# Optimization experiments

Hardware: AMD Instinct MI355X
Metric: run time of the kernel (lower is better)

## Reference

```python
import jax, jax.numpy as jnp
import numpy as np

N = 25600            # 64 graphs x 400 ROIs
F_IN = 400
H = 128
E = 512000           # 8000 edges per graph
B = 64
G = 8
OUT = 2
NPG = 400            # nodes per graph
EPG = E // B         # edges per graph
BN_EPS = 1e-5


def _xavier(k, shape):
    lim = float(np.sqrt(6.0 / (shape[0] + shape[1])))
    return jax.random.uniform(k, shape, jnp.float32, -lim, lim)


def setup_inputs() -> dict:
    key = jax.random.key(0)
    ks = jax.random.split(key, 16)
    inp = {}
    inp["x"] = jax.random.normal(ks[0], (N, F_IN), jnp.float32)
    # within-graph random edges: local index + graph offset
    src_l = jax.random.randint(ks[1], (E,), 0, NPG, jnp.int32)
    dst_l = jax.random.randint(ks[2], (E,), 0, NPG, jnp.int32)
    off = (jnp.arange(E, dtype=jnp.int32) // EPG) * NPG
    inp["edge_index"] = jnp.stack([src_l + off, dst_l + off])
    inp["batch"] = (jnp.arange(N, dtype=jnp.int32) // NPG)
    inp["group_ids"] = jax.random.randint(ks[3], (N,), 0, G, jnp.int32)
    inp["ge"] = _xavier(ks[4], (G, 2))
    inp["he"] = _xavier(ks[5], (2, 2))
    dims = [(F_IN + 4, H), (H, H), (H, H)]
    for i, (di, do) in enumerate(dims):
        k1, k2 = jax.random.split(ks[6 + i])
        inp[f"w{i}a"] = _xavier(k1, (di, do))
        inp[f"b{i}a"] = jnp.zeros((do,), jnp.float32)
        inp[f"g{i}"] = jnp.ones((do,), jnp.float32)
        inp[f"be{i}"] = jnp.zeros((do,), jnp.float32)
        inp[f"w{i}b"] = _xavier(k2, (do, do))
        inp[f"b{i}b"] = jnp.zeros((do,), jnp.float32)
    inp["wfa"] = _xavier(ks[10], (H, H))
    inp["bfa"] = jnp.zeros((H,), jnp.float32)
    inp["wfb"] = _xavier(ks[11], (H, OUT))
    inp["bfb"] = jnp.zeros((OUT,), jnp.float32)
    return inp


def _bn(h, gamma, beta):
    # BatchNorm1d in training mode: stats over node dimension
    mu = jnp.mean(h, axis=0, keepdims=True)
    var = jnp.var(h, axis=0, keepdims=True)
    return gamma * (h - mu) * jax.lax.rsqrt(var + BN_EPS) + beta


def reference(x, edge_index, batch, group_ids, ge, he,
              w0a, b0a, g0, be0, w0b, b0b,
              w1a, b1a, g1, be1, w1b, b1b,
              w2a, b2a, g2, be2, w2b, b2b,
              wfa, bfa, wfb, bfb):
    n = x.shape[0]
    hemi = jnp.arange(n) % 2                      # [1::2] = 1
    h = jnp.concatenate([x, ge[group_ids], he[hemi]], axis=-1)  # [N, F_IN+4]
    src, dst = edge_index[0], edge_index[1]
    layers = [(w0a, b0a, g0, be0, w0b, b0b),
              (w1a, b1a, g1, be1, w1b, b1b),
              (w2a, b2a, g2, be2, w2b, b2b)]
    for wa, ba, g, be, wb, bb in layers:
        # GINConv (eps=0): x_i + sum_{(j,i)} x_j, then 2-layer MLP w/ batchnorm
        agg = jax.ops.segment_sum(h[src], dst, num_segments=N)
        z = h + agg
        z = jax.nn.relu(_bn(z @ wa + ba, g, be))  # dropout = identity (eval)
        h = jax.nn.relu(z @ wb + bb)              # outer ReLU from forward()
    pooled = jax.ops.segment_sum(h, batch, num_segments=B)  # global_add_pool
    return jax.nn.relu(pooled @ wfa + bfa) @ wfb + bfb
```

## Files before the change

### kernel.cpp

```cpp
#include <hip/hip_runtime.h>

#define N_NODES 25600
#define F_IN 400
#define NE 512000
#define NB 64
#define NPG 400
#define EPG 8000
#define BN_EPS 1e-5f
#define NBLK 256

typedef __attribute__((ext_vector_type(8))) short short8;
typedef __attribute__((ext_vector_type(4))) float floatx4;
typedef unsigned short us;
typedef unsigned long long u64;

__device__ __forceinline__ unsigned short f2bf(float f) {
    unsigned int u = __float_as_uint(f);
    u += 0x7FFF + ((u >> 16) & 1);
    return (unsigned short)(u >> 16);
}
__device__ __forceinline__ float bf2f(unsigned short s) {
    return __uint_as_float((unsigned int)s << 16);
}
__device__ __forceinline__ short u8bf(unsigned v) {
    return (short)(__float_as_uint((float)v) >> 16);
}
__device__ __forceinline__ void ast64(void* p, u64 v) {
    __hip_atomic_store((u64*)p, v, __ATOMIC_RELAXED, __HIP_MEMORY_SCOPE_AGENT);
}
__device__ __forceinline__ u64 pk4(unsigned short a, unsigned short b, unsigned short c, unsigned short d) {
    return (u64)a | ((u64)b << 16) | ((u64)c << 32) | ((u64)d << 48);
}

__device__ __forceinline__ void gsync_tree(unsigned* bar, int bid, int phase) {
    __syncthreads();
    if (threadIdx.x == 0) {
        unsigned* leaf = bar + 32 + (bid >> 4) * 32;
        unsigned v = __hip_atomic_fetch_add(leaf, 1u, __ATOMIC_RELAXED, __HIP_MEMORY_SCOPE_AGENT);
        if (v == (unsigned)(phase * 16 - 1))
            __hip_atomic_fetch_add(bar, 1u, __ATOMIC_RELAXED, __HIP_MEMORY_SCOPE_AGENT);
        while (__hip_atomic_load(bar, __ATOMIC_RELAXED, __HIP_MEMORY_SCOPE_AGENT) < (unsigned)(phase * 16))
            __builtin_amdgcn_s_sleep(16);
        asm volatile("" ::: "memory");
    }
    __syncthreads();
}

__device__ __forceinline__ void gbar4(unsigned* gc, int stage) {
    __syncthreads();
    if (threadIdx.x == 0) {
        __hip_atomic_fetch_add(gc, 1u, __ATOMIC_RELAXED, __HIP_MEMORY_SCOPE_AGENT);
        while (__hip_atomic_load(gc, __ATOMIC_RELAXED, __HIP_MEMORY_SCOPE_AGENT) < (unsigned)(stage * 4))
            __builtin_amdgcn_s_sleep(8);
        asm volatile("" ::: "memory");
    }
    __syncthreads();
}



__device__ __forceinline__ void ph_prep(unsigned char* sm, int g, int q, int bid, int tid,
        const int* __restrict__ src, const int* __restrict__ dst, us* __restrict__ SbBF,
        const float* __restrict__ wa0, const float* __restrict__ wa1, const float* __restrict__ wa2,
        const float* __restrict__ wb0, const float* __restrict__ wb1, const float* __restrict__ wb2,
        us* __restrict__ wt0, us* __restrict__ wtb0, us* __restrict__ wta1,
        us* __restrict__ wtb1, us* __restrict__ wta2, us* __restrict__ wtb2,
        float* __restrict__ pstat, us* __restrict__ tT0, us* __restrict__ tT1, us* __restrict__ tT2) {
    int r0 = q * 112;
    int* cnt = (int*)sm;
    for (int i = tid; i < 11200; i += 1024) cnt[i] = 0;
    __syncthreads();
    int ebase = g * EPG, nbase = g * NPG;
    for (int e = tid; e < EPG; e += 1024) {
        int d = dst[ebase + e] - nbase;
        int dr = d - r0;
        if ((unsigned)dr < 112u) {
            int s = src[ebase + e] - nbase;
            int idx = dr * NPG + s;
            atomicAdd(&cnt[idx >> 2], (int)(1u << ((idx & 3) * 8)));
        }
    }
    __syncthreads();
    const unsigned char* cb = (const unsigned char*)cnt;
    for (int i = tid; i < 112 * 112; i += 1024) {
        int rr = i / 112, c4 = (i % 112) * 4;
        int R = r0 + rr;
        ushort4 o;
#pragma unroll
        for (int j = 0; j < 4; ++j) {
            int c = c4 + j;
            unsigned v = (R < NPG && c < NPG) ? (unsigned)cb[rr * NPG + c] + (c == R ? 1u : 0u) : 0u;
            ((unsigned short*)&o)[j] = (unsigned short)u8bf(v);
        }
        *(ushort4*)&SbBF[((size_t)g * 512 + R) * 448 + c4] = o;
    }
    if (q == 3) {
        for (int i = tid; i < 64 * 112; i += 1024) {
            int rr = 448 + i / 112, c4 = (i % 112) * 4;
            *(u64*)&SbBF[((size_t)g * 512 + rr) * 448 + c4] = 0ull;
        }
    }
    if (bid < 64) {
        int idx = bid * 1024 + tid;
        if (idx < 14336) {
            int n = idx / 112, k0 = (idx % 112) * 4;
            unsigned short o[4];
#pragma unroll
            for (int j = 0; j < 4; ++j) {
                int k = k0 + j;
                o[j] = (k < 400) ? f2bf(wa0[(size_t)k * 128 + n]) : (unsigned short)0;
            }
            ast64(&wt0[(size_t)n * 448 + k0], pk4(o[0], o[1], o[2], o[3]));
        } else if (idx < 34816) {
            int r2 = idx - 14336;
            int m = r2 >> 12, qi = r2 & 4095;
            int r = qi * 4, n = r >> 7, k = r & 127;
            const float* smat = (m == 0) ? wb0 : (m == 1) ? wa1 : (m == 2) ? wb1 : (m == 3) ? wa2 : wb2;
            us* dmat = (m == 0) ? wtb0 : (m == 1) ? wta1 : (m == 2) ? wtb1 : (m == 3) ? wta2 : wtb2;
            unsigned short o[4];
#pragma unroll
            for (int j = 0; j < 4; ++j) o[j] = f2bf(smat[(size_t)(k + j) * 128 + n]);
            ast64(&dmat[r], pk4(o[0], o[1], o[2], o[3]));
        } else if (idx < 45056) {
            int qi = idx - 34816;
            ast64(&((u64*)pstat)[qi], 0ull);
        } else if (idx < 45440) {
            int qi = idx - 45056;
            us* t = (qi < 128) ? tT0 : (qi < 256) ? tT1 : tT2;
            ast64(&t[(size_t)128 * N_NODES + (qi & 127) * 4], 0ull);
        }
    }
}


__device__ __forceinline__ void ph_embed(unsigned char* sm, int g, int q, int tid,
        const float* __restrict__ x, const us* __restrict__ wt0, const float* __restrict__ wa0,
        const int* __restrict__ gid, const float* __restrict__ ge, const float* __restrict__ he,
        us* __restrict__ tTw) {
    us (*Bf)[456] = (us(*)[456])sm;
    us (*As)[72] = (us(*)[72])(sm + 116736);
    float (*Wex)[128] = (float(*)[128])(sm + 135168);
    int nb = g * NPG + q * 100;
    int wave = tid >> 6, lane = tid & 63;
    int wrow = wave >> 2, wc4 = wave & 3;
    int fm = lane & 15, quad = lane >> 4;

    for (int i = tid; i < 7168; i += 1024) {
        int col = i / 56, kq = (i % 56) * 8;
        *(short8*)&Bf[col][kq] = *(const short8*)(wt0 + (size_t)col * 448 + kq);
    }
    for (int i = tid; i < 512; i += 1024)
        Wex[i >> 7][i & 127] = wa0[(size_t)(400 + (i >> 7)) * 128 + (i & 127)];

    floatx4 acc[2][2];
#pragma unroll
    for (int rt = 0; rt < 2; ++rt)
#pragma unroll
        for (int ct = 0; ct < 2; ++ct) acc[rt][ct] = (floatx4){0.f, 0.f, 0.f, 0.f};

    const int rA = tid >> 3, kcA = (tid & 7) * 8;
    float v[8];
    auto loadK = [&](int ks) {
        int kg = ks * 64 + kcA;
        if (rA < 100) {
            const float* ar = x + (size_t)(nb + rA) * F_IN;
            if (kg + 7 < 400) {
                float4 a = *(const float4*)(ar + kg);
                float4 b = *(const float4*)(ar + kg + 4);
                v[0] = a.x; v[1] = a.y; v[2] = a.z; v[3] = a.w;
                v[4] = b.x; v[5] = b.y; v[6] = b.z; v[7] = b.w;
            } else {
#pragma unroll
                for (int j = 0; j < 8; ++j) v[j] = (kg + j < 400) ? ar[kg + j] : 0.f;
            }
        } else {
#pragma unroll
            for (int j = 0; j < 8; ++j) v[j] = 0.f;
        }
    };

    loadK(0);
    for (int ks = 0; ks < 7; ++ks) {
        {
            short8 s;
#pragma unroll
            for (int j = 0; j < 8; ++j) s[j] = (short)f2bf(v[j]);
            *(short8*)&As[rA][kcA] = s;
        }
        __syncthreads();
        if (ks + 1 < 7) loadK(ks + 1);
#pragma unroll
        for (int k0l = 0; k0l < 64; k0l += 32) {
            short8 af[2], bf[2];
#pragma unroll
            for (int rt = 0; rt < 2; ++rt)
                af[rt] = *(const short8*)&As[wrow * 32 + rt * 16 + fm][k0l + quad * 8];
#pragma unroll
            for (int ct = 0; ct < 2; ++ct)
                bf[ct] = *(const short8*)&Bf[wc4 * 32 + ct * 16 + fm][ks * 64 + k0l + quad * 8];
#pragma unroll
            for (int rt = 0; rt < 2; ++rt)
#pragma unroll
                for (int ct = 0; ct < 2; ++ct)
                    acc[rt][ct] = __builtin_amdgcn_mfma_f32_16x16x32_bf16(
                        af[rt], bf[ct], acc[rt][ct], 0, 0, 0);
        }
        __syncthreads();
    }

#pragma unroll
    for (int rt = 0; rt < 2; ++rt)
#pragma unroll
        for (int ct = 0; ct < 2; ++ct) {
            int col = wc4 * 32 + ct * 16 + fm;
            int rl0 = wrow * 32 + rt * 16 + quad * 4;
            if (rl0 < 100) {
                unsigned short o[4];
#pragma unroll
                for (int r = 0; r < 4; ++r) {
                    int row = nb + rl0 + r;
                    int gv = gid[row];
                    float vv = acc[rt][ct][r]
                             + ge[gv * 2] * Wex[0][col] + ge[gv * 2 + 1] * Wex[1][col]
                             + he[(row & 1) * 2] * Wex[2][col] + he[(row & 1) * 2 + 1] * Wex[3][col];
                    o[r] = f2bf(vv);
                }
                ast64(&tTw[(size_t)col * N_NODES + nb + rl0], pk4(o[0], o[1], o[2], o[3]));
            }
        }
}


__device__ __forceinline__ void ph_agg(unsigned char* sm, int g, int q, int tid,
        const us* __restrict__ SbBF, const us* __restrict__ tTr, const float* __restrict__ ba,
        float* __restrict__ psum, float* __restrict__ psq, int bucket) {
    us (*Bf)[456] = (us(*)[456])sm;
    us (*zl)[136] = (us(*)[136])sm;
    float (*rs)[4][2][16] = (float(*)[4][2][16])(sm + 116736);
    float (*rq)[4][2][16] = (float(*)[4][2][16])(sm + 118784);
    int wave = tid >> 6, lane = tid & 63;
    int wrow = wave >> 2, wc4 = wave & 3;
    int fm = lane & 15, quad = lane >> 4;
    int node0 = g * NPG;

    for (int i = tid; i < 7168; i += 1024) {
        int col = i / 56, kq = (i % 56) * 8;
        *(short8*)&Bf[col][kq] = *(const short8*)(tTr + (size_t)col * N_NODES + node0 + kq);
    }
    __syncthreads();

    floatx4 acc[2][2];
#pragma unroll
    for (int rt = 0; rt < 2; ++rt)
#pragma unroll
        for (int ct = 0; ct < 2; ++ct) acc[rt][ct] = (floatx4){0.f, 0.f, 0.f, 0.f};

    const us* abase = SbBF + ((size_t)g * 512 + q * 112) * 448;
#pragma unroll
    for (int ks = 0; ks < 7; ++ks) {
#pragma unroll
        for (int k0l = 0; k0l < 64; k0l += 32) {
            short8 af[2], bf[2];
#pragma unroll
            for (int rt = 0; rt < 2; ++rt)
                af[rt] = *(const short8*)(abase + (size_t)(wrow * 32 + rt * 16 + fm) * 448
                                          + ks * 64 + k0l + quad * 8);
#pragma unroll
            for (int ct = 0; ct < 2; ++ct)
                bf[ct] = *(const short8*)&Bf[wc4 * 32 + ct * 16 + fm][ks * 64 + k0l + quad * 8];
#pragma unroll
            for (int rt = 0; rt < 2; ++rt)
#pragma unroll
                for (int ct = 0; ct < 2; ++ct)
                    acc[rt][ct] = __builtin_amdgcn_mfma_f32_16x16x32_bf16(
                        af[rt], bf[ct], acc[rt][ct], 0, 0, 0);
        }
    }
    __syncthreads();

    int nrows = (q < 3) ? 112 : 64;
    float sc[2] = {0.f, 0.f}, sq2[2] = {0.f, 0.f};
#pragma unroll
    for (int rt = 0; rt < 2; ++rt)
#pragma unroll
        for (int ct = 0; ct < 2; ++ct) {
            int col = wc4 * 32 + ct * 16 + fm;
            int rl0 = wrow * 32 + rt * 16 + quad * 4;
            if (rl0 < nrows) {
                float bv = ba[col];
#pragma unroll
                for (int r = 0; r < 4; ++r) {
                    float vv = acc[rt][ct][r] + bv;
                    zl[rl0 + r][col] = f2bf(vv);
                    sc[ct] += vv;
                    sq2[ct] += vv * vv;
                }
            }
        }
#pragma unroll
    for (int ct = 0; ct < 2; ++ct) {
        sc[ct] += __shfl_xor(sc[ct], 16);
        sc[ct] += __shfl_xor(sc[ct], 32);
        sq2[ct] += __shfl_xor(sq2[ct], 16);
        sq2[ct] += __shfl_xor(sq2[ct], 32);
    }
    if (lane < 16) {
#pragma unroll
        for (int ct = 0; ct < 2; ++ct) { rs[wrow][wc4][ct][lane] = sc[ct]; rq[wrow][wc4][ct][lane] = sq2[ct]; }
    }
    __syncthreads();
    if (tid < 128) {
        int wc = tid >> 5, ct = (tid >> 4) & 1, f = tid & 15;
        float S = 0.f, Q = 0.f;
#pragma unroll
        for (int wr = 0; wr < 4; ++wr) { S += rs[wr][wc][ct][f]; Q += rq[wr][wc][ct][f]; }
        atomicAdd(&psum[bucket * 128 + tid], S);
        atomicAdd(&psq[bucket * 128 + tid], Q);
    }
}


template <int FINAL>
__device__ __forceinline__ void ph_post(unsigned char* sm, int g, int q, int tid,
        const float* __restrict__ psum, const float* __restrict__ psq,
        const float* __restrict__ gamma, const float* __restrict__ beta,
        const us* __restrict__ wtb, const float* __restrict__ bb,
        const us* __restrict__ wta_next, us* __restrict__ tTw, float& p0, float& p1) {
    us (*zl)[136] = (us(*)[136])sm;
    float* coefs = (float*)(sm + 34816);
    us (*hs)[136] = (us(*)[136])(sm + 35840);
    us (*Bw)[72] = (us(*)[72])(sm + 70656);
    int wave = tid >> 6, lane = tid & 63;
    int wrow = wave >> 2, wc4 = wave & 3;
    int fm = lane & 15, quad = lane >> 4;
    int nrows = (q < 3) ? 112 : 64;
    int nb = g * NPG + q * 112;

    if (tid < 128) {
        float S = 0.f, Q = 0.f;
#pragma unroll
        for (int b = 0; b < 16; ++b) {
            S += __hip_atomic_load(&psum[b * 128 + tid], __ATOMIC_RELAXED, __HIP_MEMORY_SCOPE_AGENT);
            Q += __hip_atomic_load(&psq[b * 128 + tid], __ATOMIC_RELAXED, __HIP_MEMORY_SCOPE_AGENT);
        }
        float invn = 1.0f / (float)N_NODES;
        float mu = S * invn;
        float var = Q * invn - mu * mu;
        float a = gamma[tid] * rsqrtf(var + BN_EPS);
        coefs[tid] = a;
        coefs[128 + tid] = beta[tid] - a * mu;
    }
    __syncthreads();
    for (int i = tid; i < 16384; i += 1024) {
        int rl = i >> 7, col = i & 127;
        float vv = bf2f(zl[rl][col]);
        zl[rl][col] = f2bf(fmaxf(coefs[col] * vv + coefs[128 + col], 0.f));
    }
    __syncthreads();

    floatx4 acc[2][2];
#pragma unroll
    for (int rt = 0; rt < 2; ++rt)
#pragma unroll
        for (int ct = 0; ct < 2; ++ct) acc[rt][ct] = (floatx4){0.f, 0.f, 0.f, 0.f};

    const int nB = tid >> 3, kc = (tid & 7) * 8;
    for (int ks = 0; ks < 2; ++ks) {
        *(short8*)&Bw[nB][kc] = *(const short8*)(wtb + (size_t)nB * 128 + ks * 64 + kc);
        __syncthreads();
#pragma unroll
        for (int k0l = 0; k0l < 64; k0l += 32) {
            short8 af[2], bf[2];
#pragma unroll
            for (int rt = 0; rt < 2; ++rt)
                af[rt] = *(const short8*)&zl[wrow * 32 + rt * 16 + fm][ks * 64 + k0l + quad * 8];
#pragma unroll
            for (int ct = 0; ct < 2; ++ct)
                bf[ct] = *(const short8*)&Bw[wc4 * 32 + ct * 16 + fm][k0l + quad * 8];
#pragma unroll
            for (int rt = 0; rt < 2; ++rt)
#pragma unroll
                for (int ct = 0; ct < 2; ++ct)
                    acc[rt][ct] = __builtin_amdgcn_mfma_f32_16x16x32_bf16(
                        af[rt], bf[ct], acc[rt][ct], 0, 0, 0);
        }
        __syncthreads();
    }

    if (FINAL) {
#pragma unroll
        for (int rt = 0; rt < 2; ++rt)
#pragma unroll
            for (int ct = 0; ct < 2; ++ct) {
                int col = wc4 * 32 + ct * 16 + fm;
                int rl0 = wrow * 32 + rt * 16 + quad * 4;
                if (rl0 < nrows) {
                    float bv = bb[col];
                    float s = 0.f;
#pragma unroll
                    for (int r = 0; r < 4; ++r) s += fmaxf(acc[rt][ct][r] + bv, 0.f);
                    if (ct == 0) p0 += s; else p1 += s;
                }
            }
        return;
    }

#pragma unroll
    for (int rt = 0; rt < 2; ++rt)
#pragma unroll
        for (int ct = 0; ct < 2; ++ct) {
            int col = wc4 * 32 + ct * 16 + fm;
            float bv = bb[col];
            int rl0 = wrow * 32 + rt * 16 + quad * 4;
#pragma unroll
            for (int r = 0; r < 4; ++r)
                hs[rl0 + r][col] = f2bf(fmaxf(acc[rt][ct][r] + bv, 0.f));
        }
    __syncthreads();

#pragma unroll
    for (int rt = 0; rt < 2; ++rt)
#pragma unroll
        for (int ct = 0; ct < 2; ++ct) acc[rt][ct] = (floatx4){0.f, 0.f, 0.f, 0.f};

    for (int ks = 0; ks < 2; ++ks) {
        *(short8*)&Bw[nB][kc] = *(const short8*)(wta_next + (size_t)nB * 128 + ks * 64 + kc);
        __syncthreads();
#pragma unroll
        for (int k0l = 0; k0l < 64; k0l += 32) {
            short8 af[2], bf[2];
#pragma unroll
            for (int rt = 0; rt < 2; ++rt)
                af[rt] = *(const short8*)&hs[wrow * 32 + rt * 16 + fm][ks * 64 + k0l + quad * 8];
#pragma unroll
            for (int ct = 0; ct < 2; ++ct)
                bf[ct] = *(const short8*)&Bw[wc4 * 32 + ct * 16 + fm][k0l + quad * 8];
#pragma unroll
            for (int rt = 0; rt < 2; ++rt)
#pragma unroll
                for (int ct = 0; ct < 2; ++ct)
                    acc[rt][ct] = __builtin_amdgcn_mfma_f32_16x16x32_bf16(
                        af[rt], bf[ct], acc[rt][ct], 0, 0, 0);
        }
        __syncthreads();
    }

#pragma unroll
    for (int rt = 0; rt < 2; ++rt)
#pragma unroll
        for (int ct = 0; ct < 2; ++ct) {
            int col = wc4 * 32 + ct * 16 + fm;
            int rl0 = wrow * 32 + rt * 16 + quad * 4;
            if (rl0 < nrows) {
                unsigned short o[4];
#pragma unroll
                for (int r = 0; r < 4; ++r) o[r] = f2bf(acc[rt][ct][r]);
                ast64(&tTw[(size_t)col * N_NODES + nb + rl0], pk4(o[0], o[1], o[2], o[3]));
            }
        }
}


__global__ __launch_bounds__(1024, 4) void persist_all(
        const float* __restrict__ x, const int* __restrict__ esrc, const int* __restrict__ edst,
        const int* __restrict__ gid, const float* __restrict__ ge, const float* __restrict__ he,
        const float* __restrict__ wa0, const float* __restrict__ ba0, const float* __restrict__ gg0,
        const float* __restrict__ be0, const float* __restrict__ wb0, const float* __restrict__ bbias0,
        const float* __restrict__ wa1, const float* __restrict__ ba1, const float* __restrict__ gg1,
        const float* __restrict__ be1, const float* __restrict__ wb1, const float* __restrict__ bbias1,
        const float* __restrict__ wa2, const float* __restrict__ ba2, const float* __restrict__ gg2,
        const float* __restrict__ be2, const float* __restrict__ wb2, const float* __restrict__ bbias2,
        const float* __restrict__ wfa, const float* __restrict__ bfa,
        const float* __restrict__ wfb, const float* __restrict__ bfb,
        us* __restrict__ tT0, us* __restrict__ tT1, us* __restrict__ tT2,
        us* __restrict__ SbBF, float* __restrict__ pstat,
        us* __restrict__ wt0, us* __restrict__ wtb0, us* __restrict__ wta1,
        us* __restrict__ wtb1, us* __restrict__ wta2, us* __restrict__ wtb2,
        unsigned* __restrict__ bar, float* __restrict__ out) {
    __shared__ __align__(16) unsigned char sm[137216];
    int bid = blockIdx.x, tid = threadIdx.x;
    int g = (bid & 7) * 8 + ((bid >> 3) & 7);
    int q = bid >> 6;
    unsigned* gc = bar + 544 + g * 32;
    float* pooled = pstat + 12288;
    float p0 = 0.f, p1 = 0.f;

    ph_prep(sm, g, q, bid, tid, esrc, edst, SbBF, wa0, wa1, wa2, wb0, wb1, wb2,
            wt0, wtb0, wta1, wtb1, wta2, wtb2, pstat, tT0, tT1, tT2);
    gsync_tree(bar, bid, 1);
    ph_embed(sm, g, q, tid, x, wt0, wa0, gid, ge, he, tT0);
    gbar4(gc, 1);

    ph_agg(sm, g, q, tid, SbBF, tT0, ba0, pstat + 0, pstat + 2048, bid & 15);
    gsync_tree(bar, bid, 2);
    ph_post<0>(sm, g, q, tid, pstat + 0, pstat + 2048, gg0, be0, wtb0, bbias0, wta1, tT1, p0, p1);
    gbar4(gc, 2);

    ph_agg(sm, g, q, tid, SbBF, tT1, ba1, pstat + 4096, pstat + 6144, bid & 15);
    gsync_tree(bar, bid, 3);
    ph_post<0>(sm, g, q, tid, pstat + 4096, pstat + 6144, gg1, be1, wtb1, bbias1, wta2, tT2, p0, p1);
    gbar4(gc, 3);

    ph_agg(sm, g, q, tid, SbBF, tT2, ba2, pstat + 8192, pstat + 10240, bid & 15);
    gsync_tree(bar, bid, 4);
    ph_post<1>(sm, g, q, tid, pstat + 8192, pstat + 10240, gg2, be2, wtb2, bbias2, nullptr, nullptr, p0, p1);

    {
        int wave = tid >> 6, lane = tid & 63;
        int wrow = wave >> 2, wc4 = wave & 3;
        float (*red)[4][2][16] = (float(*)[4][2][16])sm;
        p0 += __shfl_xor(p0, 16); p0 += __shfl_xor(p0, 32);
        p1 += __shfl_xor(p1, 16); p1 += __shfl_xor(p1, 32);
        __syncthreads();
        if (lane < 16) { red[wrow][wc4][0][lane] = p0; red[wrow][wc4][1][lane] = p1; }
        __syncthreads();
        if (tid < 128) {
            int wc = tid >> 5, ct = (tid >> 4) & 1, f = tid & 15;
            float s = 0.f;
#pragma unroll
            for (int wr = 0; wr < 4; ++wr) s += red[wr][wc][ct][f];
            atomicAdd(&pooled[g * 128 + tid], s);
        }
    }
    gbar4(gc, 4);

    if (q == 0) {
        float* pl = (float*)sm;
        float* o0 = pl + 128;
        float* o1 = pl + 256;
        __syncthreads();
        if (tid < 128) {
            unsigned uv = __hip_atomic_load((const unsigned*)&pooled[g * 128 + tid],
                                            __ATOMIC_RELAXED, __HIP_MEMORY_SCOPE_AGENT);
            pl[tid] = __uint_as_float(uv);
        }
        __syncthreads();
        if (tid < 128) {
            float a = bfa[tid];
            for (int k = 0; k < 128; ++k) a += pl[k] * wfa[k * 128 + tid];
            float p2 = fmaxf(a, 0.f);
            o0[tid] = p2 * wfb[tid * 2 + 0];
            o1[tid] = p2 * wfb[tid * 2 + 1];
        }
        __syncthreads();
        if (tid == 0) {
            float a0 = bfb[0], a1 = bfb[1];
#pragma unroll
            for (int k = 0; k < 128; ++k) { a0 += o0[k]; a1 += o1[k]; }
            out[g * 2 + 0] = a0;
            out[g * 2 + 1] = a1;
        }
    }
}


extern "C" void kernel_launch(void* const* d_in, const int* in_sizes, int n_in,
                              void* d_out, int out_size, void* d_ws, size_t ws_size,
                              hipStream_t stream) {
    const float* x   = (const float*)d_in[0];
    const int* ei    = (const int*)d_in[1];
    const int* gid   = (const int*)d_in[3];
    const float* ge  = (const float*)d_in[4];
    const float* he  = (const float*)d_in[5];
    float* out = (float*)d_out;

    char* ws = (char*)d_ws;
    size_t o = 0;
    auto alloc = [&](size_t bytes) { char* p = ws + o; o += (bytes + 255) & ~(size_t)255; return p; };
    size_t tbytes = ((size_t)128 * N_NODES + 512) * 2;
    us* tT0 = (us*)alloc(tbytes);
    us* tT1 = (us*)alloc(tbytes);
    us* tT2 = (us*)alloc(tbytes);
    us* SbBF = (us*)alloc((size_t)NB * 512 * 448 * 2);
    float* pstat = (float*)alloc(20480 * 4);
    us* wt0  = (us*)alloc(128 * 448 * 2);
    us* wtb0 = (us*)alloc(128 * 128 * 2);
    us* wta1 = (us*)alloc(128 * 128 * 2);
    us* wtb1 = (us*)alloc(128 * 128 * 2);
    us* wta2 = (us*)alloc(128 * 128 * 2);
    us* wtb2 = (us*)alloc(128 * 128 * 2);
    unsigned* bar = (unsigned*)alloc(12288);
    (void)ws_size; (void)in_sizes; (void)n_in; (void)out_size;

    hipMemsetAsync(bar, 0, 12288, stream);

    persist_all<<<NBLK, 1024, 0, stream>>>(
        x, ei, ei + NE, gid, ge, he,
        (const float*)d_in[6],  (const float*)d_in[7],  (const float*)d_in[8],
        (const float*)d_in[9],  (const float*)d_in[10], (const float*)d_in[11],
        (const float*)d_in[12], (const float*)d_in[13], (const float*)d_in[14],
        (const float*)d_in[15], (const float*)d_in[16], (const float*)d_in[17],
        (const float*)d_in[18], (const float*)d_in[19], (const float*)d_in[20],
        (const float*)d_in[21], (const float*)d_in[22], (const float*)d_in[23],
        (const float*)d_in[24], (const float*)d_in[25],
        (const float*)d_in[26], (const float*)d_in[27],
        tT0, tT1, tT2, SbBF, pstat, wt0, wtb0, wta1, wtb1, wta2, wtb2,
        bar, out);
}
```

Measured before the change: 244.6 us.

## Batch weight prefetches, shrink adjacency buffers, and move stat zeroing to memset

Several changes land together. The pstat and barrier zeroing moves into a single hipMemsetAsync, and the weight transpose work is spread over all blocks. The padded rows of the adjacency matrix and the tail padding of the activation buffers are dropped, with guarded zero loads replacing them. LDS staging in embed and agg is batched into register prefetches, and post loads full weight matrices into LDS upfront, which removes the per-k-step syncthreads. The barrier spin sleep is also shortened. Together these aim to cut barrier and sync overhead and lower memory traffic, at the cost of more register pressure.

Measured after the change: 248.1 us. About the same (+1.4%).

```diff
diff --git a/kernel.cpp b/kernel.cpp
--- a/kernel.cpp
+++ b/kernel.cpp
@@ -40,7 +40,7 @@
         if (v == (unsigned)(phase * 16 - 1))
             __hip_atomic_fetch_add(bar, 1u, __ATOMIC_RELAXED, __HIP_MEMORY_SCOPE_AGENT);
         while (__hip_atomic_load(bar, __ATOMIC_RELAXED, __HIP_MEMORY_SCOPE_AGENT) < (unsigned)(phase * 16))
-            __builtin_amdgcn_s_sleep(16);
+            __builtin_amdgcn_s_sleep(8);
         asm volatile("" ::: "memory");
     }
     __syncthreads();
@@ -64,8 +64,7 @@
         const float* __restrict__ wa0, const float* __restrict__ wa1, const float* __restrict__ wa2,
         const float* __restrict__ wb0, const float* __restrict__ wb1, const float* __restrict__ wb2,
         us* __restrict__ wt0, us* __restrict__ wtb0, us* __restrict__ wta1,
-        us* __restrict__ wtb1, us* __restrict__ wta2, us* __restrict__ wtb2,
-        float* __restrict__ pstat, us* __restrict__ tT0, us* __restrict__ tT1, us* __restrict__ tT2) {
+        us* __restrict__ wtb1, us* __restrict__ wta2, us* __restrict__ wtb2) {
     int r0 = q * 112;
     int* cnt = (int*)sm;
     for (int i = tid; i < 11200; i += 1024) cnt[i] = 0;
@@ -92,16 +91,10 @@
             unsigned v = (R < NPG && c < NPG) ? (unsigned)cb[rr * NPG + c] + (c == R ? 1u : 0u) : 0u;
             ((unsigned short*)&o)[j] = (unsigned short)u8bf(v);
         }
-        *(ushort4*)&SbBF[((size_t)g * 512 + R) * 448 + c4] = o;
-    }
-    if (q == 3) {
-        for (int i = tid; i < 64 * 112; i += 1024) {
-            int rr = 448 + i / 112, c4 = (i % 112) * 4;
-            *(u64*)&SbBF[((size_t)g * 512 + rr) * 448 + c4] = 0ull;
-        }
-    }
-    if (bid < 64) {
-        int idx = bid * 1024 + tid;
+        *(ushort4*)&SbBF[((size_t)g * 448 + R) * 448 + c4] = o;
+    }
+    if (tid < 136) {
+        int idx = bid * 136 + tid;
         if (idx < 14336) {
             int n = idx / 112, k0 = (idx % 112) * 4;
             unsigned short o[4];
@@ -111,23 +104,16 @@
                 o[j] = (k < 400) ? f2bf(wa0[(size_t)k * 128 + n]) : (unsigned short)0;
             }
             ast64(&wt0[(size_t)n * 448 + k0], pk4(o[0], o[1], o[2], o[3]));
-        } else if (idx < 34816) {
+        } else {
             int r2 = idx - 14336;
-            int m = r2 >> 12, qi = r2 & 4095;
-            int r = qi * 4, n = r >> 7, k = r & 127;
+            int m = r2 >> 12, q2 = r2 & 4095;
+            int n = q2 >> 5, k0 = (q2 & 31) * 4;
             const float* smat = (m == 0) ? wb0 : (m == 1) ? wa1 : (m == 2) ? wb1 : (m == 3) ? wa2 : wb2;
             us* dmat = (m == 0) ? wtb0 : (m == 1) ? wta1 : (m == 2) ? wtb1 : (m == 3) ? wta2 : wtb2;
             unsigned short o[4];
 #pragma unroll
-            for (int j = 0; j < 4; ++j) o[j] = f2bf(smat[(size_t)(k + j) * 128 + n]);
-            ast64(&dmat[r], pk4(o[0], o[1], o[2], o[3]));
-        } else if (idx < 45056) {
-            int qi = idx - 34816;
-            ast64(&((u64*)pstat)[qi], 0ull);
-        } else if (idx < 45440) {
-            int qi = idx - 45056;
-            us* t = (qi < 128) ? tT0 : (qi < 256) ? tT1 : tT2;
-            ast64(&t[(size_t)128 * N_NODES + (qi & 127) * 4], 0ull);
+            for (int j = 0; j < 4; ++j) o[j] = f2bf(smat[(size_t)(k0 + j) * 128 + n]);
+            ast64(&dmat[(size_t)n * 128 + k0], pk4(o[0], o[1], o[2], o[3]));
         }
     }
 }
@@ -136,7 +122,7 @@
 __device__ __forceinline__ void ph_embed(unsigned char* sm, int g, int q, int tid,
         const float* __restrict__ x, const us* __restrict__ wt0, const float* __restrict__ wa0,
         const int* __restrict__ gid, const float* __restrict__ ge, const float* __restrict__ he,
-        us* __restrict__ tTw) {
+        us* __restrict__ tT0) {
     us (*Bf)[456] = (us(*)[456])sm;
     us (*As)[72] = (us(*)[72])(sm + 116736);
     float (*Wex)[128] = (float(*)[128])(sm + 135168);
@@ -145,9 +131,20 @@
     int wrow = wave >> 2, wc4 = wave & 3;
     int fm = lane & 15, quad = lane >> 4;
 
-    for (int i = tid; i < 7168; i += 1024) {
-        int col = i / 56, kq = (i % 56) * 8;
-        *(short8*)&Bf[col][kq] = *(const short8*)(wt0 + (size_t)col * 448 + kq);
+    {
+        short8 tp[7];
+#pragma unroll
+        for (int j = 0; j < 7; ++j) {
+            int i = tid + j * 1024;
+            int col = i / 56, kq = (i - col * 56) * 8;
+            tp[j] = *(const short8*)(wt0 + (size_t)col * 448 + kq);
+        }
+#pragma unroll
+        for (int j = 0; j < 7; ++j) {
+            int i = tid + j * 1024;
+            int col = i / 56, kq = (i - col * 56) * 8;
+            *(short8*)&Bf[col][kq] = tp[j];
+        }
     }
     for (int i = tid; i < 512; i += 1024)
         Wex[i >> 7][i & 127] = wa0[(size_t)(400 + (i >> 7)) * 128 + (i & 127)];
@@ -225,7 +222,7 @@
                              + he[(row & 1) * 2] * Wex[2][col] + he[(row & 1) * 2 + 1] * Wex[3][col];
                     o[r] = f2bf(vv);
                 }
-                ast64(&tTw[(size_t)col * N_NODES + nb + rl0], pk4(o[0], o[1], o[2], o[3]));
+                ast64(&tT0[(size_t)col * N_NODES + nb + rl0], pk4(o[0], o[1], o[2], o[3]));
             }
         }
 }
@@ -243,9 +240,21 @@
     int fm = lane & 15, quad = lane >> 4;
     int node0 = g * NPG;
 
-    for (int i = tid; i < 7168; i += 1024) {
-        int col = i / 56, kq = (i % 56) * 8;
-        *(short8*)&Bf[col][kq] = *(const short8*)(tTr + (size_t)col * N_NODES + node0 + kq);
+    {
+        short8 tp[7];
+        const short8 z8 = {0, 0, 0, 0, 0, 0, 0, 0};
+#pragma unroll
+        for (int j = 0; j < 7; ++j) {
+            int i = tid + j * 1024;
+            int col = i / 56, kq = (i - col * 56) * 8;
+            tp[j] = (kq < 400) ? *(const short8*)(tTr + (size_t)col * N_NODES + node0 + kq) : z8;
+        }
+#pragma unroll
+        for (int j = 0; j < 7; ++j) {
+            int i = tid + j * 1024;
+            int col = i / 56, kq = (i - col * 56) * 8;
+            *(short8*)&Bf[col][kq] = tp[j];
+        }
     }
     __syncthreads();
 
@@ -255,7 +264,7 @@
 #pragma unroll
         for (int ct = 0; ct < 2; ++ct) acc[rt][ct] = (floatx4){0.f, 0.f, 0.f, 0.f};
 
-    const us* abase = SbBF + ((size_t)g * 512 + q * 112) * 448;
+    const us* abase = SbBF + ((size_t)g * 448 + q * 112) * 448;
 #pragma unroll
     for (int ks = 0; ks < 7; ++ks) {
 #pragma unroll
@@ -324,17 +333,25 @@
 __device__ __forceinline__ void ph_post(unsigned char* sm, int g, int q, int tid,
         const float* __restrict__ psum, const float* __restrict__ psq,
         const float* __restrict__ gamma, const float* __restrict__ beta,
-        const us* __restrict__ wtb, const float* __restrict__ bb,
-        const us* __restrict__ wta_next, us* __restrict__ tTw, float& p0, float& p1) {
+        const us* __restrict__ wtbP, const float* __restrict__ bb,
+        const us* __restrict__ wanP, us* __restrict__ tTw, float& p0, float& p1) {
     us (*zl)[136] = (us(*)[136])sm;
     float* coefs = (float*)(sm + 34816);
-    us (*hs)[136] = (us(*)[136])(sm + 35840);
-    us (*Bw)[72] = (us(*)[72])(sm + 70656);
+    us (*Bw)[136] = (us(*)[136])(sm + 35840);
     int wave = tid >> 6, lane = tid & 63;
     int wrow = wave >> 2, wc4 = wave & 3;
     int fm = lane & 15, quad = lane >> 4;
     int nrows = (q < 3) ? 112 : 64;
     int nb = g * NPG + q * 112;
+
+    short8 w1[2], w2[2];
+#pragma unroll
+    for (int j = 0; j < 2; ++j) {
+        int i = tid + j * 1024;
+        int col = i >> 4, kq = (i & 15) * 8;
+        w1[j] = *(const short8*)(wtbP + (size_t)col * 128 + kq);
+        if (!FINAL) w2[j] = *(const short8*)(wanP + (size_t)col * 128 + kq);
+    }
 
     if (tid < 128) {
         float S = 0.f, Q = 0.f;
@@ -350,6 +367,12 @@
         coefs[tid] = a;
         coefs[128 + tid] = beta[tid] - a * mu;
     }
+#pragma unroll
+    for (int j = 0; j < 2; ++j) {
+        int i = tid + j * 1024;
+        int col = i >> 4, kq = (i & 15) * 8;
+        *(short8*)&Bw[col][kq] = w1[j];
+    }
     __syncthreads();
     for (int i = tid; i < 16384; i += 1024) {
         int rl = i >> 7, col = i & 127;
@@ -364,10 +387,8 @@
 #pragma unroll
         for (int ct = 0; ct < 2; ++ct) acc[rt][ct] = (floatx4){0.f, 0.f, 0.f, 0.f};
 
-    const int nB = tid >> 3, kc = (tid & 7) * 8;
-    for (int ks = 0; ks < 2; ++ks) {
-        *(short8*)&Bw[nB][kc] = *(const short8*)(wtb + (size_t)nB * 128 + ks * 64 + kc);
-        __syncthreads();
+#pragma unroll
+    for (int ks = 0; ks < 2; ++ks)
 #pragma unroll
         for (int k0l = 0; k0l < 64; k0l += 32) {
             short8 af[2], bf[2];
@@ -376,7 +397,7 @@
                 af[rt] = *(const short8*)&zl[wrow * 32 + rt * 16 + fm][ks * 64 + k0l + quad * 8];
 #pragma unroll
             for (int ct = 0; ct < 2; ++ct)
-                bf[ct] = *(const short8*)&Bw[wc4 * 32 + ct * 16 + fm][k0l + quad * 8];
+                bf[ct] = *(const short8*)&Bw[wc4 * 32 + ct * 16 + fm][ks * 64 + k0l + quad * 8];
 #pragma unroll
             for (int rt = 0; rt < 2; ++rt)
 #pragma unroll
@@ -384,8 +405,6 @@
                     acc[rt][ct] = __builtin_amdgcn_mfma_f32_16x16x32_bf16(
                         af[rt], bf[ct], acc[rt][ct], 0, 0, 0);
         }
-        __syncthreads();
-    }
 
     if (FINAL) {
 #pragma unroll
@@ -405,6 +424,7 @@
         return;
     }
 
+    __syncthreads();
 #pragma unroll
     for (int rt = 0; rt < 2; ++rt)
 #pragma unroll
@@ -414,8 +434,14 @@
             int rl0 = wrow * 32 + rt * 16 + quad * 4;
 #pragma unroll
             for (int r = 0; r < 4; ++r)
-                hs[rl0 + r][col] = f2bf(fmaxf(acc[rt][ct][r] + bv, 0.f));
-        }
+                zl[rl0 + r][col] = f2bf(fmaxf(acc[rt][ct][r] + bv, 0.f));
+        }
+#pragma unroll
+    for (int j = 0; j < 2; ++j) {
+        int i = tid + j * 1024;
+        int col = i >> 4, kq = (i & 15) * 8;
+        *(short8*)&Bw[col][kq] = w2[j];
+    }
     __syncthreads();
 
 #pragma unroll
@@ -423,18 +449,17 @@
 #pragma unroll
         for (int ct = 0; ct < 2; ++ct) acc[rt][ct] = (floatx4){0.f, 0.f, 0.f, 0.f};
 
-    for (int ks = 0; ks < 2; ++ks) {
-        *(short8*)&Bw[nB][kc] = *(const short8*)(wta_next + (size_t)nB * 128 + ks * 64 + kc);
-        __syncthreads();
+#pragma unroll
+    for (int ks = 0; ks < 2; ++ks)
 #pragma unroll
         for (int k0l = 0; k0l < 64; k0l += 32) {
             short8 af[2], bf[2];
 #pragma unroll
             for (int rt = 0; rt < 2; ++rt)
-                af[rt] = *(const short8*)&hs[wrow * 32 + rt * 16 + fm][ks * 64 + k0l + quad * 8];
+                af[rt] = *(const short8*)&zl[wrow * 32 + rt * 16 + fm][ks * 64 + k0l + quad * 8];
 #pragma unroll
             for (int ct = 0; ct < 2; ++ct)
-                bf[ct] = *(const short8*)&Bw[wc4 * 32 + ct * 16 + fm][k0l + quad * 8];
+                bf[ct] = *(const short8*)&Bw[wc4 * 32 + ct * 16 + fm][ks * 64 + k0l + quad * 8];
 #pragma unroll
             for (int rt = 0; rt < 2; ++rt)
 #pragma unroll
@@ -442,8 +467,6 @@
                     acc[rt][ct] = __builtin_amdgcn_mfma_f32_16x16x32_bf16(
                         af[rt], bf[ct], acc[rt][ct], 0, 0, 0);
         }
-        __syncthreads();
-    }
 
 #pragma unroll
     for (int rt = 0; rt < 2; ++rt)
@@ -473,10 +496,10 @@
         const float* __restrict__ wfa, const float* __restrict__ bfa,
         const float* __restrict__ wfb, const float* __restrict__ bfb,
         us* __restrict__ tT0, us* __restrict__ tT1, us* __restrict__ tT2,
-        us* __restrict__ SbBF, float* __restrict__ pstat,
+        us* __restrict__ SbBF, float* __restrict__ pstat, unsigned* __restrict__ bar,
         us* __restrict__ wt0, us* __restrict__ wtb0, us* __restrict__ wta1,
         us* __restrict__ wtb1, us* __restrict__ wta2, us* __restrict__ wtb2,
-        unsigned* __restrict__ bar, float* __restrict__ out) {
+        float* __restrict__ out) {
     __shared__ __align__(16) unsigned char sm[137216];
     int bid = blockIdx.x, tid = threadIdx.x;
     int g = (bid & 7) * 8 + ((bid >> 3) & 7);
@@ -486,8 +509,9 @@
     float p0 = 0.f, p1 = 0.f;
 
     ph_prep(sm, g, q, bid, tid, esrc, edst, SbBF, wa0, wa1, wa2, wb0, wb1, wb2,
-            wt0, wtb0, wta1, wtb1, wta2, wtb2, pstat, tT0, tT1, tT2);
+            wt0, wtb0, wta1, wtb1, wta2, wtb2);
     gsync_tree(bar, bid, 1);
+
     ph_embed(sm, g, q, tid, x, wt0, wa0, gid, ge, he, tT0);
     gbar4(gc, 1);
 
@@ -567,22 +591,22 @@
     char* ws = (char*)d_ws;
     size_t o = 0;
     auto alloc = [&](size_t bytes) { char* p = ws + o; o += (bytes + 255) & ~(size_t)255; return p; };
-    size_t tbytes = ((size_t)128 * N_NODES + 512) * 2;
+    size_t tbytes = (size_t)128 * N_NODES * 2;
     us* tT0 = (us*)alloc(tbytes);
     us* tT1 = (us*)alloc(tbytes);
     us* tT2 = (us*)alloc(tbytes);
-    us* SbBF = (us*)alloc((size_t)NB * 512 * 448 * 2);
+    us* SbBF = (us*)alloc((size_t)NB * 448 * 448 * 2);
     float* pstat = (float*)alloc(20480 * 4);
+    unsigned* bar = (unsigned*)alloc(12288);
     us* wt0  = (us*)alloc(128 * 448 * 2);
     us* wtb0 = (us*)alloc(128 * 128 * 2);
     us* wta1 = (us*)alloc(128 * 128 * 2);
     us* wtb1 = (us*)alloc(128 * 128 * 2);
     us* wta2 = (us*)alloc(128 * 128 * 2);
     us* wtb2 = (us*)alloc(128 * 128 * 2);
-    unsigned* bar = (unsigned*)alloc(12288);
     (void)ws_size; (void)in_sizes; (void)n_in; (void)out_size;
 
-    hipMemsetAsync(bar, 0, 12288, stream);
+    hipMemsetAsync(pstat, 0, 81920 + 12288, stream);
 
     persist_all<<<NBLK, 1024, 0, stream>>>(
         x, ei, ei + NE, gid, ge, he,
@@ -594,6 +618,7 @@
         (const float*)d_in[21], (const float*)d_in[22], (const float*)d_in[23],
         (const float*)d_in[24], (const float*)d_in[25],
         (const float*)d_in[26], (const float*)d_in[27],
-        tT0, tT1, tT2, SbBF, pstat, wt0, wtb0, wta1, wtb1, wta2, wtb2,
-        bar, out);
-}
+        tT0, tT1, tT2, SbBF, pstat, bar,
+        wt0, wtb0, wta1, wtb1, wta2, wtb2,
+        out);
+}
```
